# Performance work log

Hardware: AMD Instinct MI355X
Metric: run time of the kernel (lower is better)

The kernel has to match this reference:

```python
import jax, jax.numpy as jnp
import numpy as np

THRESHOLD = 0.05

def binarize101(w, threshold):
    # Ternary quantization to {-1, 0, +1}: zero inside the dead-zone [-thr, thr].
    pos = (w > threshold).astype(w.dtype)
    neg = (w < -threshold).astype(w.dtype)
    return pos - neg

def setup_inputs() -> dict:
    key = jax.random.key(0)
    k1, k2, k3 = jax.random.split(key, 3)
    x = jax.random.normal(k1, (8192, 4096), dtype=jnp.float32)
    weight = jax.random.normal(k2, (4096, 4096), dtype=jnp.float32)
    bias = jax.random.normal(k3, (4096,), dtype=jnp.float32)
    return {"x": x, "weight": weight, "bias": bias}

def reference(x, weight, bias):
    wb = binarize101(weight, THRESHOLD)
    # F.linear: x @ wb.T + bias ; x: [N, in], weight: [out, in] -> [N, out]
    return jnp.einsum('ni,oi->no', x, wb) + bias
```

## Files before the change

kernel.cpp:

```cpp
#include <hip/hip_runtime.h>

typedef float floatx16 __attribute__((ext_vector_type(16)));
typedef __bf16 bf16x8 __attribute__((ext_vector_type(8)));
using u16 = unsigned short;
using u32 = unsigned int;

#define GLOBAL_AS __attribute__((address_space(1)))
#define LDS_AS    __attribute__((address_space(3)))

__device__ __forceinline__ u32 rne_bf16(float f) {
  u32 u = __float_as_uint(f);
  return (u + 0x7FFFu + ((u >> 16) & 1u)) >> 16;
}

__global__ __launch_bounds__(256) void cvt_x_perm(const float* __restrict__ x,
                                                  u16* __restrict__ xb, int K) {
  __shared__ u16 sm[16384];
  const int tid = threadIdx.x;
  const int Kt = K >> 6;
  const int pn = blockIdx.x / Kt, tt = blockIdx.x % Kt;
  const float* src = x + (size_t)pn * 256 * K + tt * 64;
#pragma unroll
  for (int j = 0; j < 16; ++j) {
    const int fc = j * 256 + tid;
    const int row = fc >> 4, kl4 = fc & 15;
    const float4 v = *(const float4*)(src + (size_t)row * K + kl4 * 4);
    uint2 o;
    o.x = rne_bf16(v.x) | (rne_bf16(v.y) << 16);
    o.y = rne_bf16(v.z) | (rne_bf16(v.w) << 16);
    const int gi = row >> 5, rowin = row & 31;
    const int ks = kl4 >> 2;
    const int lane = rowin + 32 * ((kl4 >> 1) & 1);
    const int e4 = (kl4 & 1) * 4;
    *(uint2*)(sm + gi * 2048 + ks * 512 + lane * 8 + e4) = o;
  }
  __syncthreads();
  u16* dst = xb + (size_t)pn * 256 * K + (size_t)tt * 16384;
#pragma unroll
  for (int j = 0; j < 8; ++j) {
    const int o = (j * 256 + tid) * 8;
    *(uint4*)(dst + o) = *(const uint4*)(sm + o);
  }
}

__global__ __launch_bounds__(256) void quant_w_perm(const float* __restrict__ w,
                                                    u16* __restrict__ wb, int K) {
  __shared__ u16 sm[16384];
  const int tid = threadIdx.x;
  const int Kt = K >> 6;
  const int pn = blockIdx.x / Kt, tt = blockIdx.x % Kt;
  const float* src = w + (size_t)pn * 256 * K + tt * 64;
#pragma unroll
  for (int j = 0; j < 16; ++j) {
    const int fc = j * 256 + tid;
    const int row = fc >> 4, kl4 = fc & 15;
    const float4 v = *(const float4*)(src + (size_t)row * K + kl4 * 4);
    float vv[4] = {v.x, v.y, v.z, v.w};
    u32 r[4];
#pragma unroll
    for (int e = 0; e < 4; ++e)
      r[e] = (vv[e] > 0.05f) ? 0x3F80u : ((vv[e] < -0.05f) ? 0xBF80u : 0u);
    uint2 o;
    o.x = r[0] | (r[1] << 16);
    o.y = r[2] | (r[3] << 16);
    const int gi = row >> 5, rowin = row & 31;
    const int ks = kl4 >> 2;
    const int lane = rowin + 32 * ((kl4 >> 1) & 1);
    const int e4 = (kl4 & 1) * 4;
    *(uint2*)(sm + gi * 2048 + ks * 512 + lane * 8 + e4) = o;
  }
  __syncthreads();
  u16* dst = wb + (size_t)pn * 256 * K + (size_t)tt * 16384;
#pragma unroll
  for (int j = 0; j < 8; ++j) {
    const int o = (j * 256 + tid) * 8;
    *(uint4*)(dst + o) = *(const uint4*)(sm + o);
  }
}

__global__ __launch_bounds__(512, 2) void gemm_bin_csched(
    const u16* __restrict__ Ap, const u16* __restrict__ Bp,
    const float* __restrict__ bias, float* __restrict__ C,
    int M, int N, int K) {
  __shared__ u16 lds[65536];

  const int tid = threadIdx.x;
  const int w = tid >> 6, l = tid & 63;
  const int wr = w >> 2, wc = w & 3;

  const int nbn = N >> 8;
  int wg = blockIdx.x;
  const int nwg = gridDim.x;
  if ((nwg & 7) == 0) wg = (wg & 7) * (nwg >> 3) + (wg >> 3);
  const int bm = wg / nbn, bn = wg % nbn;

  const int T = K >> 6;

  const u16* const Abase = Ap + (size_t)bm * ((size_t)K << 8) + tid * 8;
  const u16* const Bbase = Bp + (size_t)bn * ((size_t)K << 8) + tid * 8;

  const u16* const afp0 = lds + wr * 8192 + l * 8;
  const u16* const bfp0 = lds + 16384 + wc * 4096 + l * 8;

  floatx16 acc[4][2] = {};
  bf16x8 af[8], af2[8], bflo[4], bfhi[4];

#define GLOAD(gptr, u16off)                                                    \
  __builtin_amdgcn_global_load_lds((const GLOBAL_AS void*)(gptr),              \
                                   (LDS_AS void*)(lds + (u16off)), 16, 0, 0)
#define STAGE8(tt, bufdst)                                                     \
  {                                                                            \
    const size_t tb_ = (size_t)(tt) * 16384;                                   \
    GLOAD(Abase + tb_ + 0 * 4096, (bufdst) + 0 + tid * 8);                     \
    GLOAD(Abase + tb_ + 1 * 4096, (bufdst) + 4096 + tid * 8);                  \
    GLOAD(Abase + tb_ + 2 * 4096, (bufdst) + 8192 + tid * 8);                  \
    GLOAD(Abase + tb_ + 3 * 4096, (bufdst) + 12288 + tid * 8);                 \
    GLOAD(Bbase + tb_ + 0 * 4096, (bufdst) + 16384 + tid * 8);                 \
    GLOAD(Bbase + tb_ + 1 * 4096, (bufdst) + 20480 + tid * 8);                 \
    GLOAD(Bbase + tb_ + 2 * 4096, (bufdst) + 24576 + tid * 8);                 \
    GLOAD(Bbase + tb_ + 3 * 4096, (bufdst) + 28672 + tid * 8);                 \
  }
#define SYNC_TILE asm volatile("s_waitcnt vmcnt(0) lgkmcnt(0)\ns_barrier" ::: "memory")

  STAGE8(0, 0)
  SYNC_TILE;

  for (int t = 0; t < T; ++t) {
    const int bufc = (t & 1) << 15;
    const int bufo = bufc ^ 32768;
    const bool st1 = (t + 1 < T);

    if (st1) STAGE8(t + 1, bufo)

    const u16* afp = afp0 + bufc;
    const u16* bfp = bfp0 + bufc;

#pragma unroll
    for (int m = 0; m < 2; ++m)
#pragma unroll
      for (int ks = 0; ks < 4; ++ks)
        af[m * 4 + ks] = *(const bf16x8*)(afp + m * 2048 + ks * 512);
#pragma unroll
    for (int ks = 0; ks < 4; ++ks) bflo[ks] = *(const bf16x8*)(bfp + ks * 512);
#pragma unroll
    for (int ks = 0; ks < 4; ++ks) bfhi[ks] = *(const bf16x8*)(bfp + 2048 + ks * 512);
#pragma unroll
    for (int m = 0; m < 2; ++m)
#pragma unroll
      for (int ks = 0; ks < 4; ++ks)
        af2[m * 4 + ks] = *(const bf16x8*)(afp + 4096 + m * 2048 + ks * 512);

#pragma unroll
    for (int ks = 0; ks < 4; ++ks)
#pragma unroll
      for (int m = 0; m < 2; ++m)
        acc[m][0] = __builtin_amdgcn_mfma_f32_32x32x16_bf16(
            af[m * 4 + ks], bflo[ks], acc[m][0], 0, 0, 0);
#pragma unroll
    for (int ks = 0; ks < 4; ++ks)
#pragma unroll
      for (int m = 0; m < 2; ++m)
        acc[m][1] = __builtin_amdgcn_mfma_f32_32x32x16_bf16(
            af[m * 4 + ks], bfhi[ks], acc[m][1], 0, 0, 0);
#pragma unroll
    for (int ks = 0; ks < 4; ++ks)
#pragma unroll
      for (int m = 0; m < 2; ++m)
        acc[2 + m][0] = __builtin_amdgcn_mfma_f32_32x32x16_bf16(
            af2[m * 4 + ks], bflo[ks], acc[2 + m][0], 0, 0, 0);
#pragma unroll
    for (int ks = 0; ks < 4; ++ks)
#pragma unroll
      for (int m = 0; m < 2; ++m)
        acc[2 + m][1] = __builtin_amdgcn_mfma_f32_32x32x16_bf16(
            af2[m * 4 + ks], bfhi[ks], acc[2 + m][1], 0, 0, 0);

    if (st1) SYNC_TILE;
  }
#undef STAGE8
#undef GLOAD
#undef SYNC_TILE

  const int colq = l & 31;
  const int hi4 = (l >> 5) * 4;
#pragma unroll
  for (int m = 0; m < 4; ++m) {
    const int rowb = bm * 256 + wr * 128 + m * 32 + hi4;
#pragma unroll
    for (int n = 0; n < 2; ++n) {
      const int col = bn * 256 + wc * 64 + n * 32 + colq;
      const float bv = bias[col];
      float* cp = C + (size_t)rowb * N + col;
#pragma unroll
      for (int q = 0; q < 16; ++q) {
        const int dr = (q & 3) + 8 * (q >> 2);
        cp[(size_t)dr * N] = acc[m][n][q] + bv;
      }
    }
  }
}

__global__ void gemm_naive_kernel(const float* __restrict__ x, const float* __restrict__ wgt,
                                  const float* __restrict__ bias, float* __restrict__ out,
                                  int M, int N, int K) {
  long long idx = (long long)blockIdx.x * blockDim.x + threadIdx.x;
  if (idx >= (long long)M * N) return;
  int o = (int)(idx % N);
  int m = (int)(idx / N);
  const float* xr = x + (size_t)m * K;
  const float* wr = wgt + (size_t)o * K;
  float s = 0.f;
  for (int i = 0; i < K; ++i) {
    float wv = wr[i];
    float t = (wv > 0.05f) ? 1.f : ((wv < -0.05f) ? -1.f : 0.f);
    s = fmaf(xr[i], t, s);
  }
  out[idx] = s + bias[o];
}

extern "C" void kernel_launch(void* const* d_in, const int* in_sizes, int n_in,
                              void* d_out, int out_size, void* d_ws, size_t ws_size,
                              hipStream_t stream) {
  const float* x    = (const float*)d_in[0];
  const float* wgt  = (const float*)d_in[1];
  const float* bias = (const float*)d_in[2];
  float* out = (float*)d_out;

  const int N = in_sizes[2];
  const int K = in_sizes[1] / N;
  const int M = in_sizes[0] / K;

  const size_t need = ((size_t)M * K + (size_t)N * K) * sizeof(u16);
  if (ws_size >= need && (M % 256 == 0) && (N % 256 == 0) && (K % 64 == 0) && K >= 192) {
    u16* xb = (u16*)d_ws;
    u16* wb = xb + (size_t)M * K;
    const int Kt = K / 64;
    cvt_x_perm<<<(M / 256) * Kt, 256, 0, stream>>>(x, xb, K);
    quant_w_perm<<<(N / 256) * Kt, 256, 0, stream>>>(wgt, wb, K);
    const int grid = (M / 256) * (N / 256);
    gemm_bin_csched<<<grid, 512, 0, stream>>>(xb, wb, bias, out, M, N, K);
  } else {
    const long long total = (long long)M * N;
    gemm_naive_kernel<<<(unsigned)((total + 255) / 256), 256, 0, stream>>>(x, wgt, bias, out, M, N, K);
  }
}
```

Measured before the change: 288.8 us.

## Load B fragments directly from global into registers, bypassing LDS

Re-lays out the quantized weight so each wave's B fragments are contiguous per k-tile, then loads B straight from global memory into registers with prefetch of the next tile interleaved between MFMA groups. Only A is staged through LDS, halving the LDS footprint and the LDS read traffic for B. The trade-off is that B is now fetched redundantly by the two wave rows, adds register pressure, and relies on hand-tuned vmcnt waits to hide global latency.

```diff
diff --git a/kernel.cpp b/kernel.cpp
--- a/kernel.cpp
+++ b/kernel.cpp
@@ -43,8 +43,8 @@
   }
 }
 
-__global__ __launch_bounds__(256) void quant_w_perm(const float* __restrict__ w,
-                                                    u16* __restrict__ wb, int K) {
+__global__ __launch_bounds__(256) void quant_w_permB(const float* __restrict__ w,
+                                                     u16* __restrict__ wb, int K) {
   __shared__ u16 sm[16384];
   const int tid = threadIdx.x;
   const int Kt = K >> 6;
@@ -63,26 +63,26 @@
     uint2 o;
     o.x = r[0] | (r[1] << 16);
     o.y = r[2] | (r[3] << 16);
-    const int gi = row >> 5, rowin = row & 31;
-    const int ks = kl4 >> 2;
-    const int lane = rowin + 32 * ((kl4 >> 1) & 1);
-    const int e4 = (kl4 & 1) * 4;
-    *(uint2*)(sm + gi * 2048 + ks * 512 + lane * 8 + e4) = o;
+    const int wc = row >> 6, ng = (row >> 5) & 1, cf = row & 31;
+    const int ks = kl4 >> 2, hi = (kl4 >> 1) & 1, e4 = (kl4 & 1) * 4;
+    const int f = ng * 4 + ks, l = cf + 32 * hi;
+    *(uint2*)(sm + wc * 4096 + f * 512 + l * 8 + e4) = o;
   }
   __syncthreads();
-  u16* dst = wb + (size_t)pn * 256 * K + (size_t)tt * 16384;
 #pragma unroll
   for (int j = 0; j < 8; ++j) {
-    const int o = (j * 256 + tid) * 8;
-    *(uint4*)(dst + o) = *(const uint4*)(sm + o);
-  }
-}
-
-__global__ __launch_bounds__(512, 2) void gemm_bin_csched(
+    const int o16 = (j * 256 + tid) * 8;
+    const int wco = o16 >> 12, inner = o16 & 4095;
+    u16* dst = wb + ((size_t)(pn * 4 + wco) * Kt + tt) * 4096 + inner;
+    *(uint4*)dst = *(const uint4*)(sm + o16);
+  }
+}
+
+__global__ __launch_bounds__(512, 2) void gemm_bin_breg2(
     const u16* __restrict__ Ap, const u16* __restrict__ Bp,
     const float* __restrict__ bias, float* __restrict__ C,
     int M, int N, int K) {
-  __shared__ u16 lds[65536];
+  __shared__ u16 lds[32768];
 
   const int tid = threadIdx.x;
   const int w = tid >> 6, l = tid & 63;
@@ -97,10 +97,9 @@
   const int T = K >> 6;
 
   const u16* const Abase = Ap + (size_t)bm * ((size_t)K << 8) + tid * 8;
-  const u16* const Bbase = Bp + (size_t)bn * ((size_t)K << 8) + tid * 8;
+  const u16* const Bbase = Bp + ((size_t)(bn * 4 + wc) * T) * 4096 + l * 8;
 
   const u16* const afp0 = lds + wr * 8192 + l * 8;
-  const u16* const bfp0 = lds + 16384 + wc * 4096 + l * 8;
 
   floatx16 acc[4][2] = {};
   bf16x8 af[8], af2[8], bflo[4], bfhi[4];
@@ -108,42 +107,40 @@
 #define GLOAD(gptr, u16off)                                                    \
   __builtin_amdgcn_global_load_lds((const GLOBAL_AS void*)(gptr),              \
                                    (LDS_AS void*)(lds + (u16off)), 16, 0, 0)
-#define STAGE8(tt, bufdst)                                                     \
+#define ASTAGE(tt, bufdst)                                                     \
   {                                                                            \
     const size_t tb_ = (size_t)(tt) * 16384;                                   \
     GLOAD(Abase + tb_ + 0 * 4096, (bufdst) + 0 + tid * 8);                     \
     GLOAD(Abase + tb_ + 1 * 4096, (bufdst) + 4096 + tid * 8);                  \
     GLOAD(Abase + tb_ + 2 * 4096, (bufdst) + 8192 + tid * 8);                  \
     GLOAD(Abase + tb_ + 3 * 4096, (bufdst) + 12288 + tid * 8);                 \
-    GLOAD(Bbase + tb_ + 0 * 4096, (bufdst) + 16384 + tid * 8);                 \
-    GLOAD(Bbase + tb_ + 1 * 4096, (bufdst) + 20480 + tid * 8);                 \
-    GLOAD(Bbase + tb_ + 2 * 4096, (bufdst) + 24576 + tid * 8);                 \
-    GLOAD(Bbase + tb_ + 3 * 4096, (bufdst) + 28672 + tid * 8);                 \
-  }
-#define SYNC_TILE asm volatile("s_waitcnt vmcnt(0) lgkmcnt(0)\ns_barrier" ::: "memory")
-
-  STAGE8(0, 0)
-  SYNC_TILE;
+  }
+
+  ASTAGE(0, 0)
+  __builtin_amdgcn_sched_barrier(0);
+#pragma unroll
+  for (int ks = 0; ks < 4; ++ks)
+    bflo[ks] = *(const bf16x8*)(Bbase + ks * 512);
+#pragma unroll
+  for (int ks = 0; ks < 4; ++ks)
+    bfhi[ks] = *(const bf16x8*)(Bbase + (4 + ks) * 512);
+  asm volatile("s_waitcnt vmcnt(8)\ns_barrier" ::: "memory");
 
   for (int t = 0; t < T; ++t) {
-    const int bufc = (t & 1) << 15;
-    const int bufo = bufc ^ 32768;
+    const int bufc = (t & 1) << 14;
+    const int bufo = bufc ^ 16384;
     const bool st1 = (t + 1 < T);
-
-    if (st1) STAGE8(t + 1, bufo)
-
     const u16* afp = afp0 + bufc;
-    const u16* bfp = bfp0 + bufc;
+    const u16* Bnext = Bbase + (size_t)(t + 1) * 4096;
+
+    if (st1) ASTAGE(t + 1, bufo)
+    __builtin_amdgcn_sched_barrier(0);
 
 #pragma unroll
     for (int m = 0; m < 2; ++m)
 #pragma unroll
       for (int ks = 0; ks < 4; ++ks)
         af[m * 4 + ks] = *(const bf16x8*)(afp + m * 2048 + ks * 512);
-#pragma unroll
-    for (int ks = 0; ks < 4; ++ks) bflo[ks] = *(const bf16x8*)(bfp + ks * 512);
-#pragma unroll
-    for (int ks = 0; ks < 4; ++ks) bfhi[ks] = *(const bf16x8*)(bfp + 2048 + ks * 512);
 #pragma unroll
     for (int m = 0; m < 2; ++m)
 #pragma unroll
@@ -160,26 +157,38 @@
     for (int ks = 0; ks < 4; ++ks)
 #pragma unroll
       for (int m = 0; m < 2; ++m)
+        acc[2 + m][0] = __builtin_amdgcn_mfma_f32_32x32x16_bf16(
+            af2[m * 4 + ks], bflo[ks], acc[2 + m][0], 0, 0, 0);
+
+    if (st1) {
+#pragma unroll
+      for (int ks = 0; ks < 4; ++ks)
+        bflo[ks] = *(const bf16x8*)(Bnext + ks * 512);
+      __builtin_amdgcn_sched_barrier(0);
+    }
+
+#pragma unroll
+    for (int ks = 0; ks < 4; ++ks)
+#pragma unroll
+      for (int m = 0; m < 2; ++m)
         acc[m][1] = __builtin_amdgcn_mfma_f32_32x32x16_bf16(
             af[m * 4 + ks], bfhi[ks], acc[m][1], 0, 0, 0);
 #pragma unroll
     for (int ks = 0; ks < 4; ++ks)
 #pragma unroll
       for (int m = 0; m < 2; ++m)
-        acc[2 + m][0] = __builtin_amdgcn_mfma_f32_32x32x16_bf16(
-            af2[m * 4 + ks], bflo[ks], acc[2 + m][0], 0, 0, 0);
-#pragma unroll
-    for (int ks = 0; ks < 4; ++ks)
-#pragma unroll
-      for (int m = 0; m < 2; ++m)
         acc[2 + m][1] = __builtin_amdgcn_mfma_f32_32x32x16_bf16(
             af2[m * 4 + ks], bfhi[ks], acc[2 + m][1], 0, 0, 0);
 
-    if (st1) SYNC_TILE;
-  }
-#undef STAGE8
+    if (st1) {
+#pragma unroll
+      for (int ks = 0; ks < 4; ++ks)
+        bfhi[ks] = *(const bf16x8*)(Bnext + (4 + ks) * 512);
+      asm volatile("s_waitcnt vmcnt(8)\ns_barrier" ::: "memory");
+    }
+  }
+#undef ASTAGE
 #undef GLOAD
-#undef SYNC_TILE
 
   const int colq = l & 31;
   const int hi4 = (l >> 5) * 4;
@@ -236,9 +245,9 @@
     u16* wb = xb + (size_t)M * K;
     const int Kt = K / 64;
     cvt_x_perm<<<(M / 256) * Kt, 256, 0, stream>>>(x, xb, K);
-    quant_w_perm<<<(N / 256) * Kt, 256, 0, stream>>>(wgt, wb, K);
+    quant_w_permB<<<(N / 256) * Kt, 256, 0, stream>>>(wgt, wb, K);
     const int grid = (M / 256) * (N / 256);
-    gemm_bin_csched<<<grid, 512, 0, stream>>>(xb, wb, bias, out, M, N, K);
+    gemm_bin_breg2<<<grid, 512, 0, stream>>>(xb, wb, bias, out, M, N, K);
   } else {
     const long long total = (long long)M * N;
     gemm_naive_kernel<<<(unsigned)((total + 255) / 256), 256, 0, stream>>>(x, wgt, bias, out, M, N, K);
```

Measured after the change: 294.5 us. About the same (+2.0%).
